# Kernel tuning notes

Measured on AMD Instinct MI355X. Metric: run time of the kernel, lower is better.

## Reference

```python
import jax, jax.numpy as jnp
import numpy as np

CONF_THRES = 0.5
IOU_THRES = 0.4
MAX_DET = 100
MAX_WH = 1024.0
K_NMS = 4096  # static cap on NMS candidates (>> expected #candidates passing conf_thres)


def setup_inputs() -> dict:
    key = jax.random.key(0)
    k1, k2, k3, k4 = jax.random.split(key, 4)
    bs, gs, nc = 16, 25200, 80  # YOLOv5 @ 640x640: 25200 anchors, 80 classes, ps = 85
    xy = jax.random.uniform(k1, (bs, gs, 2)) * 608.0 + 16.0   # centers in [16, 624)
    wh = jax.random.uniform(k2, (bs, gs, 2)) * 96.0 + 4.0     # sizes in [4, 100)
    obj = jax.random.uniform(k3, (bs, gs, 1))                 # objectness
    cls = jax.random.uniform(k4, (bs, gs, nc)) * 0.505        # class probs; obj*cls > 0.5 is rare (~1-2k hits)
    prediction = jnp.concatenate([xy, wh, obj, cls], axis=-1)  # [bs, gs, 85]
    return {"prediction": prediction}


def _postprocess(prediction):
    bs, gs, ps = prediction.shape
    nc = ps - 5
    p = prediction.reshape(-1, ps)                 # [N, ps], N = bs*gs
    obj = p[:, 4]                                  # objectness
    scores_all = p[:, 5:] * obj[:, None]           # conf = cls * obj, [N, nc]
    # candidate (anchor, class) pairs: obj > conf_thres AND conf > conf_thres (multi_label)
    cand = (obj[:, None] > CONF_THRES) & (scores_all > CONF_THRES)
    flat = jnp.where(cand, scores_all, -1.0).reshape(-1)       # [N*nc]
    top_scores, top_idx = jax.lax.top_k(flat, K_NMS)           # descending score order (= torch nms sort order)
    row = top_idx // nc                                        # anchor index into p
    cls_j = top_idx % nc                                       # class index
    batch = row // gs                                          # image index
    valid = top_scores > CONF_THRES

    # xywh -> xyxy
    xywh = p[row, :4]                                          # [K, 4]
    half = xywh[:, 2:4] * 0.5
    box = jnp.concatenate([xywh[:, 0:2] - half, xywh[:, 0:2] + half], axis=1)
    f32 = box.dtype

    # class-offset + batch-offset trick: c1 = batch*max_cls_idx*max_wh, c2 = class*max_wh
    offset = (batch.astype(f32) * (nc * MAX_WH) + cls_j.astype(f32) * MAX_WH)[:, None]
    nb = box + offset                                          # offset boxes for NMS

    # pairwise IoU [K, K]
    area = (nb[:, 2] - nb[:, 0]) * (nb[:, 3] - nb[:, 1])
    ix = jnp.maximum(jnp.minimum(nb[:, None, 2], nb[None, :, 2]) - jnp.maximum(nb[:, None, 0], nb[None, :, 0]), 0.0)
    iy = jnp.maximum(jnp.minimum(nb[:, None, 3], nb[None, :, 3]) - jnp.maximum(nb[:, None, 1], nb[None, :, 1]), 0.0)
    inter = ix * iy
    iou = inter / (area[:, None] + area[None, :] - inter)

    # greedy NMS over score-sorted candidates (torchvision semantics: suppress if IoU > thres)
    def step(supp, xs):
        iou_i, v_i, i = xs
        keep_i = v_i & jnp.logical_not(supp[i])
        supp = supp | (keep_i & (iou_i > IOU_THRES))
        return supp, keep_i
    _, keep = jax.lax.scan(step, jnp.zeros(K_NMS, bool), (iou, valid, jnp.arange(K_NMS)))

    # output rows: [x1, y1, x2, y2, conf, class, batch]
    rows7 = jnp.concatenate(
        [box, top_scores[:, None], cls_j.astype(f32)[:, None], batch.astype(f32)[:, None]], axis=1)

    # per-image gather of kept rows (score order), truncated to MAX_DET, zero-padded
    def gather_b(b):
        m = keep & (batch == b)
        rank = jnp.cumsum(m.astype(jnp.int32)) - 1
        idx = jnp.where(m & (rank < MAX_DET), rank, MAX_DET)   # overflow/invalid -> dropped slot
        buf = jnp.zeros((MAX_DET + 1, 7), f32).at[idx].set(jnp.where(m[:, None], rows7, 0.0))
        return buf[:MAX_DET]
    return jax.vmap(gather_b)(jnp.arange(bs))                  # [bs, MAX_DET, 7]


def reference(prediction):
    return _postprocess(prediction)
```

## Files before the change

### kernel.cpp

```cpp
#include <hip/hip_runtime.h>
#include <stdint.h>

#define BS 16
#define GS 25200
#define NC 80
#define PS 85
#define NROWS (BS * GS)
#define MAXDET 100
#define CAP 4096
#define NGROUPS (BS * NC)

struct Ws {
  int      count;
  int      keep[CAP];
  float    sc[CAP];
  int      ti[CAP];
  uint16_t gg[CAP];
  float    x1[CAP];
  float    y1[CAP];
  float    x2[CAP];
  float    y2[CAP];
};

__device__ __forceinline__ void commit(Ws* __restrict__ w,
                                       const float* __restrict__ p,
                                       int row, int c, float s, bool laneok) {
  int lane = threadIdx.x & 63;
  bool hit = laneok && (s > 0.5f);
  uint64_t mm = __ballot(hit);
  if (!mm) return;
  int leader = __ffsll((unsigned long long)mm) - 1;
  int pos0;
  if (lane == leader) pos0 = atomicAdd(&w->count, __popcll(mm));
  pos0 = __shfl(pos0, leader);
  if (hit) {
    int slot = pos0 + __popcll(mm & ((1ull << lane) - 1ull));
    if (slot < CAP) {
      const float* pr = p + (size_t)row * PS;
      float x = pr[0], y = pr[1], wd = pr[2], ht = pr[3];
      float hw = wd * 0.5f, hh = ht * 0.5f;
      int b = row / GS;
      w->sc[slot] = s;
      w->ti[slot] = row * NC + c;
      w->gg[slot] = (uint16_t)(b * NC + c);
      w->x1[slot] = x - hw;
      w->y1[slot] = y - hh;
      w->x2[slot] = x + hw;
      w->y2[slot] = y + hh;
    }
  }
}

__global__ __launch_bounds__(256) void extract_k(const float* __restrict__ p,
                                                 Ws* __restrict__ w) {
  int wv   = (blockIdx.x * 256 + threadIdx.x) >> 6;
  int lane = threadIdx.x & 63;
  int base = wv * 64;
  float obj = p[(size_t)(base + lane) * PS + 4];
  uint64_t mask = __ballot(obj > 0.5f);
  while (mask) {
    int m0 = __ffsll((unsigned long long)mask) - 1;
    mask &= mask - 1;
    int m1 = -1;
    if (mask) {
      m1 = __ffsll((unsigned long long)mask) - 1;
      mask &= mask - 1;
    }
    float ob0 = __shfl(obj, m0);
    const float* pr0 = p + (size_t)(base + m0) * PS;
    float v0a = pr0[5 + lane];
    float v0b = (lane < 16) ? pr0[69 + lane] : 0.0f;
    float ob1 = 0.0f, v1a = 0.0f, v1b = 0.0f;
    if (m1 >= 0) {
      ob1 = __shfl(obj, m1);
      const float* pr1 = p + (size_t)(base + m1) * PS;
      v1a = pr1[5 + lane];
      v1b = (lane < 16) ? pr1[69 + lane] : 0.0f;
    }
    commit(w, p, base + m0, lane,      v0a * ob0, true);
    commit(w, p, base + m0, 64 + lane, v0b * ob0, lane < 16);
    if (m1 >= 0) {
      commit(w, p, base + m1, lane,      v1a * ob1, true);
      commit(w, p, base + m1, 64 + lane, v1b * ob1, lane < 16);
    }
  }
}

__global__ __launch_bounds__(256) void nms_k(Ws* __restrict__ w) {
  __shared__ uint64_t lkey[4][64];
  __shared__ int      lj[4][64];
  int wslot = threadIdx.x >> 6;
  int wid   = (blockIdx.x * 256 + threadIdx.x) >> 6;
  int lane  = threadIdx.x & 63;
  int b = wid / NC, c = wid - b * NC;
  float offf = (float)b * (NC * 1024.0f) + (float)c * 1024.0f;
  int n = w->count;
  if (n > CAP) n = CAP;
  int nm = 0;
  for (int j0 = 0; j0 < n; j0 += 64) {
    int j = j0 + lane;
    int g = (j < n) ? (int)w->gg[j] : -1;
    bool mem = (g == wid);
    uint64_t mm = __ballot(mem);
    if (!mm) continue;
    if (mem) {
      int pos = nm + __popcll(mm & ((1ull << lane) - 1ull));
      if (pos < 64) {
        uint32_t sb = __float_as_uint(w->sc[j]);
        lkey[wslot][pos] = ((uint64_t)sb << 32) | (uint32_t)(~(uint32_t)w->ti[j]);
        lj[wslot][pos]   = j;
      } else {
        w->keep[j] = 0;
      }
    }
    nm += __popcll(mm);
  }
  __syncthreads();
  if (nm > 64) nm = 64;
  if (nm == 0) return;
  uint64_t key = (lane < nm) ? lkey[wslot][lane] : 0ull;
  int      jv  = (lane < nm) ? lj[wslot][lane] : -1;
  for (int k = 2; k <= 64; k <<= 1) {
    for (int s = k >> 1; s > 0; s >>= 1) {
      uint64_t ok = __shfl_xor(key, s);
      int      oj = __shfl_xor(jv, s);
      bool iLow       = (lane & s) == 0;
      bool descRun    = (lane & k) == 0;
      bool wantLarger = (iLow == descRun);
      bool take = wantLarger ? (ok > key) : (ok < key);
      if (take) { key = ok; jv = oj; }
    }
  }
  float kx1 = 0.f, ky1 = 0.f, kx2 = 0.f, ky2 = 0.f, ka = 0.f;
  int nk = 0;
  for (int i = 0; i < nm; ++i) {
    int jm = __shfl(jv, i);
    float cx1 = w->x1[jm] + offf;
    float cy1 = w->y1[jm] + offf;
    float cx2 = w->x2[jm] + offf;
    float cy2 = w->y2[jm] + offf;
    float car = (cx2 - cx1) * (cy2 - cy1);
    bool over = false;
    if (lane < nk) {
      float ix = fmaxf(fminf(kx2, cx2) - fmaxf(kx1, cx1), 0.0f);
      float iy = fmaxf(fminf(ky2, cy2) - fmaxf(ky1, cy1), 0.0f);
      float inter = ix * iy;
      over = inter / (ka + car - inter) > 0.4f;
    }
    bool kept = !__any(over);
    if (kept) {
      if (lane == nk) { kx1 = cx1; ky1 = cy1; kx2 = cx2; ky2 = cy2; ka = car; }
      ++nk;
    }
    if (lane == 0) w->keep[jm] = kept ? 1 : 0;
  }
}

__global__ __launch_bounds__(1024) void gather_k(const Ws* __restrict__ w,
                                                 float* __restrict__ out) {
  __shared__ uint64_t skey[BS][256];
  __shared__ int      sj[BS][256];
  int wvb  = threadIdx.x >> 6;
  int lane = threadIdx.x & 63;
  int glo = wvb * NC;
  int n = w->count;
  if (n > CAP) n = CAP;
  int nkept = 0;
  for (int j0 = 0; j0 < n; j0 += 64) {
    int j = j0 + lane;
    bool m = false;
    if (j < n) {
      int g = (int)w->gg[j];
      m = ((unsigned)(g - glo) < (unsigned)NC) && (w->keep[j] != 0);
    }
    uint64_t mm = __ballot(m);
    if (m) {
      int pos = nkept + __popcll(mm & ((1ull << lane) - 1ull));
      if (pos < 256) {
        uint32_t sb = __float_as_uint(w->sc[j]);
        skey[wvb][pos] = ((uint64_t)sb << 32) | (uint32_t)(~(uint32_t)w->ti[j]);
        sj[wvb][pos]   = j;
      }
    }
    nkept += __popcll(mm);
  }
  if (nkept > 256) nkept = 256;
  for (int e = lane; e < 256; e += 64)
    if (e >= nkept) { skey[wvb][e] = 0ull; sj[wvb][e] = -1; }
  __syncthreads();
  for (int k = 2; k <= 256; k <<= 1) {
    for (int s = k >> 1; s > 0; s >>= 1) {
      for (int e = lane; e < 256; e += 64) {
        int x = e ^ s;
        if (x > e) {
          uint64_t a = skey[wvb][e], bb = skey[wvb][x];
          bool desc = (e & k) == 0;
          if (desc ? (a < bb) : (a > bb)) {
            skey[wvb][e] = bb; skey[wvb][x] = a;
            int t = sj[wvb][e]; sj[wvb][e] = sj[wvb][x]; sj[wvb][x] = t;
          }
        }
      }
      __syncthreads();
    }
  }
  int nout = nkept < MAXDET ? nkept : MAXDET;
  float* ob = out + (size_t)wvb * MAXDET * 7;
  for (int i = lane; i < MAXDET; i += 64) {
    if (i < nout) {
      int j = sj[wvb][i];
      ob[i * 7 + 0] = w->x1[j];
      ob[i * 7 + 1] = w->y1[j];
      ob[i * 7 + 2] = w->x2[j];
      ob[i * 7 + 3] = w->y2[j];
      ob[i * 7 + 4] = w->sc[j];
      ob[i * 7 + 5] = (float)((int)w->gg[j] - glo);
      ob[i * 7 + 6] = (float)wvb;
    } else {
      for (int q = 0; q < 7; ++q) ob[i * 7 + q] = 0.0f;
    }
  }
}

extern "C" void kernel_launch(void* const* d_in, const int* in_sizes, int n_in,
                              void* d_out, int out_size, void* d_ws,
                              size_t ws_size, hipStream_t stream) {
  const float* p = (const float*)d_in[0];
  float* out = (float*)d_out;
  Ws* w = (Ws*)d_ws;

  hipMemsetAsync(&w->count, 0, sizeof(int), stream);
  hipLaunchKernelGGL(extract_k, dim3(NROWS / 64 / 4), dim3(256), 0, stream, p, w);
  hipLaunchKernelGGL(nms_k, dim3(NGROUPS / 4), dim3(256), 0, stream, w);
  hipLaunchKernelGGL(gather_k, dim3(1), dim3(1024), 0, stream, w, out);
}
```

Baseline: 102.8 us.

## Stage 64-row prediction slabs in LDS with float4 loads in extract kernel

The extract kernel now copies each contiguous 64-row block of predictions into shared memory using coalesced float4 loads. It then scans every (row, class) pair from LDS with one thread per pair instead of looping per wave over rows that pass the objectness test. The old path did strided 4-byte obj loads and then gathered per row. The new path reads the whole tensor densely, about 137 MB, where the old one read only obj and the passing rows. Grid size grows from 1575 to 6300 blocks, each holding a 21.7 KB slab.

```diff
diff --git a/kernel.cpp b/kernel.cpp
--- a/kernel.cpp
+++ b/kernel.cpp
@@ -9,6 +9,9 @@
 #define MAXDET 100
 #define CAP 4096
 #define NGROUPS (BS * NC)
+#define RPB 64
+#define SLABF (RPB * PS)
+#define PPB (RPB * NC)
 
 struct Ws {
   int      count;
@@ -22,66 +25,55 @@
   float    y2[CAP];
 };
 
-__device__ __forceinline__ void commit(Ws* __restrict__ w,
-                                       const float* __restrict__ p,
-                                       int row, int c, float s, bool laneok) {
-  int lane = threadIdx.x & 63;
-  bool hit = laneok && (s > 0.5f);
-  uint64_t mm = __ballot(hit);
-  if (!mm) return;
-  int leader = __ffsll((unsigned long long)mm) - 1;
-  int pos0;
-  if (lane == leader) pos0 = atomicAdd(&w->count, __popcll(mm));
-  pos0 = __shfl(pos0, leader);
-  if (hit) {
-    int slot = pos0 + __popcll(mm & ((1ull << lane) - 1ull));
-    if (slot < CAP) {
-      const float* pr = p + (size_t)row * PS;
-      float x = pr[0], y = pr[1], wd = pr[2], ht = pr[3];
-      float hw = wd * 0.5f, hh = ht * 0.5f;
-      int b = row / GS;
-      w->sc[slot] = s;
-      w->ti[slot] = row * NC + c;
-      w->gg[slot] = (uint16_t)(b * NC + c);
-      w->x1[slot] = x - hw;
-      w->y1[slot] = y - hh;
-      w->x2[slot] = x + hw;
-      w->y2[slot] = y + hh;
-    }
-  }
-}
-
 __global__ __launch_bounds__(256) void extract_k(const float* __restrict__ p,
                                                  Ws* __restrict__ w) {
-  int wv   = (blockIdx.x * 256 + threadIdx.x) >> 6;
-  int lane = threadIdx.x & 63;
-  int base = wv * 64;
-  float obj = p[(size_t)(base + lane) * PS + 4];
-  uint64_t mask = __ballot(obj > 0.5f);
-  while (mask) {
-    int m0 = __ffsll((unsigned long long)mask) - 1;
-    mask &= mask - 1;
-    int m1 = -1;
-    if (mask) {
-      m1 = __ffsll((unsigned long long)mask) - 1;
-      mask &= mask - 1;
-    }
-    float ob0 = __shfl(obj, m0);
-    const float* pr0 = p + (size_t)(base + m0) * PS;
-    float v0a = pr0[5 + lane];
-    float v0b = (lane < 16) ? pr0[69 + lane] : 0.0f;
-    float ob1 = 0.0f, v1a = 0.0f, v1b = 0.0f;
-    if (m1 >= 0) {
-      ob1 = __shfl(obj, m1);
-      const float* pr1 = p + (size_t)(base + m1) * PS;
-      v1a = pr1[5 + lane];
-      v1b = (lane < 16) ? pr1[69 + lane] : 0.0f;
-    }
-    commit(w, p, base + m0, lane,      v0a * ob0, true);
-    commit(w, p, base + m0, 64 + lane, v0b * ob0, lane < 16);
-    if (m1 >= 0) {
-      commit(w, p, base + m1, lane,      v1a * ob1, true);
-      commit(w, p, base + m1, 64 + lane, v1b * ob1, lane < 16);
+  __shared__ float slab[SLABF];
+  int tid = threadIdx.x;
+  const float4* __restrict__ src =
+      (const float4*)(p + (size_t)blockIdx.x * SLABF);
+  float4* dst = (float4*)slab;
+#pragma unroll
+  for (int i = 0; i < 6; ++i) {
+    int idx = tid + i * 256;
+    if (idx < SLABF / 4) dst[idx] = src[idx];
+  }
+  __syncthreads();
+  int lane = tid & 63;
+  int rowbase = blockIdx.x * RPB;
+#pragma unroll 4
+  for (int step = 0; step < PPB / 256; ++step) {
+    int k = tid + step * 256;
+    int row = k / NC;
+    int c   = k - row * NC;
+    float obj = slab[row * PS + 4];
+    bool hit = false;
+    float s = 0.0f;
+    if (obj > 0.5f) {
+      s = slab[row * PS + 5 + c] * obj;
+      hit = s > 0.5f;
+    }
+    uint64_t mm = __ballot(hit);
+    if (mm) {
+      int leader = __ffsll((unsigned long long)mm) - 1;
+      int pos0;
+      if (lane == leader) pos0 = atomicAdd(&w->count, __popcll(mm));
+      pos0 = __shfl(pos0, leader);
+      if (hit) {
+        int slot = pos0 + __popcll(mm & ((1ull << lane) - 1ull));
+        if (slot < CAP) {
+          int grow = rowbase + row;
+          int b = grow / GS;
+          float x = slab[row * PS + 0], y = slab[row * PS + 1];
+          float hw = slab[row * PS + 2] * 0.5f, hh = slab[row * PS + 3] * 0.5f;
+          w->sc[slot] = s;
+          w->ti[slot] = grow * NC + c;
+          w->gg[slot] = (uint16_t)(b * NC + c);
+          w->x1[slot] = x - hw;
+          w->y1[slot] = y - hh;
+          w->x2[slot] = x + hw;
+          w->y2[slot] = y + hh;
+        }
+      }
     }
   }
 }
@@ -230,7 +222,7 @@
   Ws* w = (Ws*)d_ws;
 
   hipMemsetAsync(&w->count, 0, sizeof(int), stream);
-  hipLaunchKernelGGL(extract_k, dim3(NROWS / 64 / 4), dim3(256), 0, stream, p, w);
+  hipLaunchKernelGGL(extract_k, dim3(NROWS / RPB), dim3(256), 0, stream, p, w);
   hipLaunchKernelGGL(nms_k, dim3(NGROUPS / 4), dim3(256), 0, stream, w);
   hipLaunchKernelGGL(gather_k, dim3(1), dim3(1024), 0, stream, w, out);
 }
```

Result: faster. 97.10 us (-5.5%).
